# Kernel tuning notes

Measured on AMD Instinct MI355X. Metric: run time of the kernel, lower is better.

## Reference

```python
import jax, jax.numpy as jnp
import numpy as np

DIM = 1024
NUM_HEADS = 16
HEAD_DIM = DIM // NUM_HEADS
SCALE = 1.0 / float(np.sqrt(HEAD_DIM))


def setup_inputs() -> dict:
    key = jax.random.key(0)
    ks = jax.random.split(key, 8)
    b, n = 1, 4096
    x = jax.random.normal(ks[0], (b, n, DIM), dtype=jnp.float32)
    cos = jax.random.uniform(ks[1], (b, n, HEAD_DIM // 2), dtype=jnp.float32)
    sin = jax.random.uniform(ks[2], (b, n, HEAD_DIM // 2), dtype=jnp.float32)
    # qkv Linear(dim, 3*dim) and proj Linear(dim, dim); store weights as [in, out]
    w_qkv = jax.random.normal(ks[3], (DIM, 3 * DIM), dtype=jnp.float32) * (1.0 / np.sqrt(DIM))
    b_qkv = jax.random.normal(ks[4], (3 * DIM,), dtype=jnp.float32) * 0.01
    w_proj = jax.random.normal(ks[5], (DIM, DIM), dtype=jnp.float32) * (1.0 / np.sqrt(DIM))
    b_proj = jax.random.normal(ks[6], (DIM,), dtype=jnp.float32) * 0.01
    return {"x": x, "cos": cos, "sin": sin, "w_qkv": w_qkv, "b_qkv": b_qkv,
            "w_proj": w_proj, "b_proj": b_proj}


def _rotate_half(t):
    t1, t2 = jnp.split(t, 2, axis=-1)
    return jnp.concatenate([-t2, t1], axis=-1)


def reference(x, cos, sin, w_qkv, b_qkv, w_proj, b_proj):
    b, n, d = x.shape
    qkv = x @ w_qkv + b_qkv                      # [b, n, 3d]
    q, k, v = jnp.split(qkv, 3, axis=-1)
    # [b, n, h, hd] layout (avoids explicit transposes; einsum handles head axis)
    q = q.reshape(b, n, NUM_HEADS, HEAD_DIM)
    k = k.reshape(b, n, NUM_HEADS, HEAD_DIM)
    v = v.reshape(b, n, NUM_HEADS, HEAD_DIM)
    # RoPE: cos/sin [b, n, hd/2] -> [b, n, 1, hd], broadcast over heads
    cos_f = jnp.concatenate([cos, cos], axis=-1)[:, :, None, :]
    sin_f = jnp.concatenate([sin, sin], axis=-1)[:, :, None, :]
    q = q * cos_f + _rotate_half(q) * sin_f
    k = k * cos_f + _rotate_half(k) * sin_f
    # SDPA (non-causal, no dropout in eval)
    scores = jnp.einsum("bqhd,bkhd->bhqk", q, k) * SCALE
    attn = jax.nn.softmax(scores, axis=-1)
    out = jnp.einsum("bhqk,bkhd->bqhd", attn, v).reshape(b, n, d)
    return out @ w_proj + b_proj
```

## Files before the change

### kernel.cpp

```cpp
#include <hip/hip_runtime.h>
#include <hip/hip_bf16.h>
#include <cstdint>


#define TOK 4096
#define DIM_ 1024
#define NHEAD 16
#define HDIM 64
#define N3 3072
#define SCALE_LOG2E 0.18033688011112042f

typedef __bf16 bf16_t;
typedef bf16_t bf16x8 __attribute__((ext_vector_type(8)));
typedef float floatx4 __attribute__((ext_vector_type(4)));

__device__ __forceinline__ void async_ld16(const bf16_t* g, bf16_t* l) {
  __builtin_amdgcn_global_load_lds(
      (const __attribute__((address_space(1))) void*)(g),
      (__attribute__((address_space(3))) void*)(l), 16, 0, 0);
}

__global__ __launch_bounds__(256) void k_prep(
    const float* __restrict__ x, const float* __restrict__ w_qkv,
    const float* __restrict__ w_proj, bf16_t* __restrict__ xb,
    bf16_t* __restrict__ wqkvT, bf16_t* __restrict__ wprojT) {
  __shared__ float tile[32][33];
  const int b = blockIdx.x;
  if (b < 4096) {
    int i = b * 256 + threadIdx.x;
    float4 v = ((const float4*)x)[i];
    union { bf16_t bb[4]; uint64_t u; } p;
    p.bb[0] = (bf16_t)v.x; p.bb[1] = (bf16_t)v.y;
    p.bb[2] = (bf16_t)v.z; p.bb[3] = (bf16_t)v.w;
    ((uint64_t*)xb)[i] = p.u;
    return;
  }
  const float* in; bf16_t* out; int R, C, c0, r0;
  if (b < 7168) {
    int bb = b - 4096; in = w_qkv; out = wqkvT; R = 1024; C = 3072;
    c0 = (bb % 96) * 32; r0 = (bb / 96) * 32;
  } else {
    int bb = b - 7168; in = w_proj; out = wprojT; R = 1024; C = 1024;
    c0 = (bb % 32) * 32; r0 = (bb / 32) * 32;
  }
  int tx = threadIdx.x & 31, ty = threadIdx.x >> 5;
#pragma unroll
  for (int i = 0; i < 4; i++) {
    int r = ty + i * 8;
    tile[r][tx] = in[(size_t)(r0 + r) * C + c0 + tx];
  }
  __syncthreads();
#pragma unroll
  for (int i = 0; i < 4; i++) {
    int c = ty + i * 8;
    out[(size_t)(c0 + c) * R + r0 + tx] = (bf16_t)tile[tx][c];
  }
}

__global__ __launch_bounds__(256) void k_qkv(
    const bf16_t* __restrict__ A,
    const bf16_t* __restrict__ Bt,
    const float* __restrict__ bias,
    const float* __restrict__ cs,
    const float* __restrict__ sn,
    bf16_t* __restrict__ qb, bf16_t* __restrict__ kb, bf16_t* __restrict__ vT) {
  constexpr int K = 1024, BK = 32;
  __shared__ bf16_t As[128 * BK] __attribute__((aligned(16)));
  __shared__ bf16_t Bs[128 * BK] __attribute__((aligned(16)));
  const int t = threadIdx.x;
  const int lane = t & 63, w = t >> 6;
  const int lrow = lane & 15, quad = lane >> 4;
  const int m0 = blockIdx.y * 128, n0 = blockIdx.x * 128;
  const int wm = (w >> 1) * 64, wn = (w & 1) * 64;

  const floatx4 ZV = {0.f, 0.f, 0.f, 0.f};
  floatx4 acc[4][4];
#pragma unroll
  for (int i = 0; i < 4; i++)
#pragma unroll
    for (int j = 0; j < 4; j++) acc[i][j] = ZV;

  for (int kt = 0; kt < K; kt += BK) {
#pragma unroll
    for (int r = 0; r < 2; r++) {
      int idx = r * 256 + t;
      int lbase = (r * 256 + w * 64) * 8;
      async_ld16(&A[(size_t)(m0 + (idx >> 2)) * K + kt + (idx & 3) * 8], &As[lbase]);
      async_ld16(&Bt[(size_t)(n0 + (idx >> 2)) * K + kt + (idx & 3) * 8], &Bs[lbase]);
    }
    __syncthreads();
    bf16x8 af[4], bf[4];
#pragma unroll
    for (int i = 0; i < 4; i++)
      af[i] = *(const bf16x8*)&As[(wm + i * 16 + lrow) * BK + quad * 8];
#pragma unroll
    for (int i = 0; i < 4; i++)
      bf[i] = *(const bf16x8*)&Bs[(wn + i * 16 + lrow) * BK + quad * 8];
#pragma unroll
    for (int mi = 0; mi < 4; mi++)
#pragma unroll
      for (int ni = 0; ni < 4; ni++)
        acc[mi][ni] = __builtin_amdgcn_mfma_f32_16x16x32_bf16(af[mi], bf[ni], acc[mi][ni], 0, 0, 0);
    __syncthreads();
  }

  const int c0 = n0 + wn;
  const int seg = c0 >> 10;
  const int h = (c0 & 1023) >> 6;
  float bv[4];
#pragma unroll
  for (int ni = 0; ni < 4; ni++) bv[ni] = bias[c0 + ni * 16 + lrow];

  if (seg < 2) {
    bf16_t* base = ((seg == 0) ? qb : kb) + (size_t)h * TOK * HDIM;
    const float qs = (seg == 0) ? SCALE_LOG2E : 1.0f;
#pragma unroll
    for (int mi = 0; mi < 4; mi++) {
#pragma unroll
      for (int reg = 0; reg < 4; reg++) {
        const int r = m0 + wm + mi * 16 + quad * 4 + reg;
        const float c_lo = cs[r * 32 + lrow];
        const float c_hi = cs[r * 32 + 16 + lrow];
        const float s_lo = sn[r * 32 + lrow];
        const float s_hi = sn[r * 32 + 16 + lrow];
        const float v0 = acc[mi][0][reg] + bv[0];
        const float v1 = acc[mi][1][reg] + bv[1];
        const float v2 = acc[mi][2][reg] + bv[2];
        const float v3 = acc[mi][3][reg] + bv[3];
        const float o0 = (v0 * c_lo - v2 * s_lo) * qs;
        const float o1 = (v1 * c_hi - v3 * s_hi) * qs;
        const float o2 = (v2 * c_lo + v0 * s_lo) * qs;
        const float o3 = (v3 * c_hi + v1 * s_hi) * qs;
        bf16_t* rp = base + (size_t)r * HDIM + lrow;
        rp[0]  = (bf16_t)o0;
        rp[16] = (bf16_t)o1;
        rp[32] = (bf16_t)o2;
        rp[48] = (bf16_t)o3;
      }
    }
  } else {
    bf16_t* base = vT + (size_t)h * HDIM * TOK;
#pragma unroll
    for (int mi = 0; mi < 4; mi++) {
      const int rbase = m0 + wm + mi * 16 + quad * 4;
#pragma unroll
      for (int ni = 0; ni < 4; ni++) {
        union { bf16_t b[4]; uint64_t u; } p;
#pragma unroll
        for (int reg = 0; reg < 4; reg++) p.b[reg] = (bf16_t)(acc[mi][ni][reg] + bv[ni]);
        *(uint64_t*)&base[(size_t)(ni * 16 + lrow) * TOK + rbase] = p.u;
      }
    }
  }
}

__global__ __launch_bounds__(256, 4) void k_attn(
    const bf16_t* __restrict__ qb, const bf16_t* __restrict__ kb,
    const bf16_t* __restrict__ vT, bf16_t* __restrict__ ao) {
  __shared__ bf16_t Ks[2][64 * 64] __attribute__((aligned(16)));
  __shared__ bf16_t Ps[4][32 * 36] __attribute__((aligned(16)));
  const int t = threadIdx.x, lane = t & 63, w = t >> 6;
  const int lrow = lane & 15, quad = lane >> 4;
  const int qg = w & 1, kh = w >> 1;
  const int bx = blockIdx.x;
  const int h = ((bx & 7) << 1) | ((bx >> 3) & 1);
  const int q0 = (bx >> 4) * 64;
  const bf16_t* qh = qb + (size_t)h * TOK * HDIM;
  const bf16_t* khp = kb + (size_t)h * TOK * HDIM;
  const bf16_t* vhp = vT + (size_t)h * HDIM * TOK;
  bf16_t* Pw = &Ps[w][0];

  const int ksrc = (t >> 3) * HDIM + (((t & 7) ^ ((t >> 3) & 7)) * 8);

  bf16x8 qf[2][2];
#pragma unroll
  for (int ni = 0; ni < 2; ni++)
#pragma unroll
    for (int ks = 0; ks < 2; ks++)
      qf[ni][ks] = *(const bf16x8*)&qh[(size_t)(q0 + qg * 32 + ni * 16 + lrow) * HDIM + ks * 32 + quad * 8];

  const floatx4 ZV = {0.f, 0.f, 0.f, 0.f};
  floatx4 o[4][2];
  floatx4 lacc[2] = {ZV, ZV};
#pragma unroll
  for (int d = 0; d < 4; d++)
#pragma unroll
    for (int ni = 0; ni < 2; ni++) o[d][ni] = ZV;

#pragma unroll
  for (int r = 0; r < 2; r++)
    async_ld16(&khp[(size_t)(r * 32) * HDIM + ksrc], &Ks[0][r * 2048 + t * 8]);

  for (int it = 0; it < TOK / 64; ++it) {
    const int b = it & 1;
    __syncthreads();
    if (it + 1 < TOK / 64) {
      const size_t j1 = (size_t)(it + 1) * 64;
#pragma unroll
      for (int r = 0; r < 2; r++)
        async_ld16(&khp[(j1 + r * 32) * HDIM + ksrc], &Ks[b ^ 1][r * 2048 + t * 8]);
    }

    bf16x8 vf[4];
#pragma unroll
    for (int dt = 0; dt < 4; dt++)
      vf[dt] = *(const bf16x8*)&vhp[(size_t)(dt * 16 + lrow) * TOK + it * 64 + kh * 32 + quad * 8];

    floatx4 s[2][2];
#pragma unroll
    for (int mi = 0; mi < 2; mi++)
#pragma unroll
      for (int ni = 0; ni < 2; ni++) s[mi][ni] = ZV;
#pragma unroll
    for (int ks = 0; ks < 2; ks++)
#pragma unroll
      for (int mi = 0; mi < 2; mi++) {
        bf16x8 kf = *(const bf16x8*)&Ks[b][(kh * 32 + mi * 16 + lrow) * 64 + (((ks * 4 + quad) ^ (lrow & 7)) * 8)];
#pragma unroll
        for (int ni = 0; ni < 2; ni++)
          s[mi][ni] = __builtin_amdgcn_mfma_f32_16x16x32_bf16(kf, qf[ni][ks], s[mi][ni], 0, 0, 0);
      }

#pragma unroll
    for (int mi = 0; mi < 2; mi++)
#pragma unroll
      for (int ni = 0; ni < 2; ni++) {
#pragma unroll
        for (int reg = 0; reg < 4; reg++)
          s[mi][ni][reg] = __builtin_amdgcn_exp2f(s[mi][ni][reg]);
        lacc[ni] += s[mi][ni];
      }

#pragma unroll
    for (int mi = 0; mi < 2; mi++)
#pragma unroll
      for (int ni = 0; ni < 2; ni++) {
        union { bf16_t b4[4]; uint64_t u; } p;
#pragma unroll
        for (int reg = 0; reg < 4; reg++) p.b4[reg] = (bf16_t)s[mi][ni][reg];
        *(uint64_t*)&Pw[(ni * 16 + lrow) * 36 + (mi * 4 + quad) * 4] = p.u;
      }

    bf16x8 pf[2];
#pragma unroll
    for (int ni = 0; ni < 2; ni++) {
      const int row = (ni * 16 + lrow) * 36;
      union { uint64_t u[2]; bf16x8 v; } pp;
      pp.u[0] = *(const uint64_t*)&Pw[row + quad * 8];
      pp.u[1] = *(const uint64_t*)&Pw[row + quad * 8 + 4];
      pf[ni] = pp.v;
    }
#pragma unroll
    for (int dt = 0; dt < 4; dt++)
#pragma unroll
      for (int ni = 0; ni < 2; ni++)
        o[dt][ni] = __builtin_amdgcn_mfma_f32_16x16x32_bf16(vf[dt], pf[ni], o[dt][ni], 0, 0, 0);
  }

  __syncthreads();
  float* Mrg = (float*)&Ks[qg][0];
  float* Lmrg = (float*)&Ps[0][0];
  float lq[2];
#pragma unroll
  for (int ni = 0; ni < 2; ni++) {
    float l = lacc[ni][0] + lacc[ni][1] + lacc[ni][2] + lacc[ni][3];
    l += __shfl_xor(l, 16, 64);
    l += __shfl_xor(l, 32, 64);
    lq[ni] = l;
  }
  if (kh == 1) {
#pragma unroll
    for (int ni = 0; ni < 2; ni++) {
#pragma unroll
      for (int dt = 0; dt < 4; dt++)
        *(floatx4*)&Mrg[(ni * 16 + lrow) * 64 + dt * 16 + quad * 4] = o[dt][ni];
      if (quad == 0) Lmrg[qg * 32 + ni * 16 + lrow] = lq[ni];
    }
  }
  __syncthreads();
  if (kh == 0) {
#pragma unroll
    for (int ni = 0; ni < 2; ni++) {
      const float l = lq[ni] + Lmrg[qg * 32 + ni * 16 + lrow];
      const float inv = 1.0f / l;
      const int qrow = q0 + qg * 32 + ni * 16 + lrow;
#pragma unroll
      for (int dt = 0; dt < 4; dt++) {
        floatx4 ov = *(const floatx4*)&Mrg[(ni * 16 + lrow) * 64 + dt * 16 + quad * 4];
        union { bf16_t b4[4]; uint64_t u; } p;
#pragma unroll
        for (int reg = 0; reg < 4; reg++) p.b4[reg] = (bf16_t)((o[dt][ni][reg] + ov[reg]) * inv);
        *(uint64_t*)&ao[(size_t)qrow * DIM_ + h * HDIM + dt * 16 + quad * 4] = p.u;
      }
    }
  }
}

__global__ __launch_bounds__(256) void k_proj(
    const bf16_t* __restrict__ A,
    const bf16_t* __restrict__ Bt,
    const float* __restrict__ bias, float* __restrict__ out) {
  constexpr int K = 1024, BK = 32;
  __shared__ bf16_t As[64 * BK] __attribute__((aligned(16)));
  __shared__ bf16_t Bs[128 * BK] __attribute__((aligned(16)));
  const int t = threadIdx.x;
  const int lane = t & 63, w = t >> 6;
  const int lrow = lane & 15, quad = lane >> 4;
  const int m0 = blockIdx.y * 64, n0 = blockIdx.x * 128;
  const int wm = (w >> 1) * 32, wn = (w & 1) * 64;

  const floatx4 ZV = {0.f, 0.f, 0.f, 0.f};
  floatx4 acc[2][4];
#pragma unroll
  for (int i = 0; i < 2; i++)
#pragma unroll
    for (int j = 0; j < 4; j++) acc[i][j] = ZV;

  for (int kt = 0; kt < K; kt += BK) {
    async_ld16(&A[(size_t)(m0 + (t >> 2)) * K + kt + (t & 3) * 8], &As[w * 512]);
#pragma unroll
    for (int r = 0; r < 2; r++) {
      int idx = r * 256 + t;
      async_ld16(&Bt[(size_t)(n0 + (idx >> 2)) * K + kt + (idx & 3) * 8],
                 &Bs[(r * 256 + w * 64) * 8]);
    }
    __syncthreads();
    bf16x8 af[2], bf[4];
#pragma unroll
    for (int i = 0; i < 2; i++)
      af[i] = *(const bf16x8*)&As[(wm + i * 16 + lrow) * BK + quad * 8];
#pragma unroll
    for (int i = 0; i < 4; i++)
      bf[i] = *(const bf16x8*)&Bs[(wn + i * 16 + lrow) * BK + quad * 8];
#pragma unroll
    for (int mi = 0; mi < 2; mi++)
#pragma unroll
      for (int ni = 0; ni < 4; ni++)
        acc[mi][ni] = __builtin_amdgcn_mfma_f32_16x16x32_bf16(af[mi], bf[ni], acc[mi][ni], 0, 0, 0);
    __syncthreads();
  }

  const int c0 = n0 + wn;
#pragma unroll
  for (int ni = 0; ni < 4; ni++) {
    float bv = bias[c0 + ni * 16 + lrow];
#pragma unroll
    for (int mi = 0; mi < 2; mi++)
#pragma unroll
      for (int reg = 0; reg < 4; reg++) {
        int r = m0 + wm + mi * 16 + quad * 4 + reg;
        out[(size_t)r * DIM_ + c0 + ni * 16 + lrow] = acc[mi][ni][reg] + bv;
      }
  }
}

extern "C" void kernel_launch(void* const* d_in, const int* in_sizes, int n_in,
                              void* d_out, int out_size, void* d_ws, size_t ws_size,
                              hipStream_t stream) {
  const float* x      = (const float*)d_in[0];
  const float* cs     = (const float*)d_in[1];
  const float* sn     = (const float*)d_in[2];
  const float* w_qkv  = (const float*)d_in[3];
  const float* b_qkv  = (const float*)d_in[4];
  const float* w_proj = (const float*)d_in[5];
  const float* b_proj = (const float*)d_in[6];
  float* out = (float*)d_out;

  char* ws = (char*)d_ws;
  bf16_t* xb     = (bf16_t*)(ws);
  bf16_t* wqkvT  = (bf16_t*)(ws + 8388608);
  bf16_t* wprojT = (bf16_t*)(ws + 14680064);
  bf16_t* qb     = (bf16_t*)(ws + 16777216);
  bf16_t* kb     = (bf16_t*)(ws + 25165824);
  bf16_t* vT     = (bf16_t*)(ws + 33554432);
  bf16_t* ao     = xb;

  k_prep<<<dim3(8192), dim3(256), 0, stream>>>(x, w_qkv, w_proj, xb, wqkvT, wprojT);
  k_qkv<<<dim3(24, 32), dim3(256), 0, stream>>>(xb, wqkvT, b_qkv, cs, sn, qb, kb, vT);
  k_attn<<<dim3(1024), dim3(256), 0, stream>>>(qb, kb, vT, ao);
  k_proj<<<dim3(8, 64), dim3(256), 0, stream>>>(ao, wprojT, b_proj, out);
}
```

Before: 277.0 us.

## Stage V through LDS, swap P via permlane, software-pipeline PV MFMA

V tiles now go into double-buffered LDS with async global-to-LDS loads, the same way K tiles do, replacing direct per-lane global loads. The bf16 P fragment is rearranged into MFMA operand layout with permlane32/permlane16 swaps instead of a round trip through per-wave LDS scratch. The PV MFMA is deferred one iteration so it overlaps the next QK and exp work, with setprio raised around the MFMA blocks. The head-to-block mapping is also simplified. This adds LDS footprint and register pressure, which may lower occupancy.

```diff
diff --git a/kernel.cpp b/kernel.cpp
--- a/kernel.cpp
+++ b/kernel.cpp
@@ -18,6 +18,12 @@
   __builtin_amdgcn_global_load_lds(
       (const __attribute__((address_space(1))) void*)(g),
       (__attribute__((address_space(3))) void*)(l), 16, 0, 0);
+}
+
+__device__ __forceinline__ uint32_t pk2(float lo, float hi) {
+  union { bf16_t b[2]; uint32_t u; } p;
+  p.b[0] = (bf16_t)lo; p.b[1] = (bf16_t)hi;
+  return p.u;
 }
 
 __global__ __launch_bounds__(256) void k_prep(
@@ -158,19 +164,19 @@
     const bf16_t* __restrict__ qb, const bf16_t* __restrict__ kb,
     const bf16_t* __restrict__ vT, bf16_t* __restrict__ ao) {
   __shared__ bf16_t Ks[2][64 * 64] __attribute__((aligned(16)));
-  __shared__ bf16_t Ps[4][32 * 36] __attribute__((aligned(16)));
+  __shared__ bf16_t Vs[2][64 * 64] __attribute__((aligned(16)));
+  __shared__ float Lmrg[64];
   const int t = threadIdx.x, lane = t & 63, w = t >> 6;
   const int lrow = lane & 15, quad = lane >> 4;
   const int qg = w & 1, kh = w >> 1;
-  const int bx = blockIdx.x;
-  const int h = ((bx & 7) << 1) | ((bx >> 3) & 1);
-  const int q0 = (bx >> 4) * 64;
+  const int h = blockIdx.x & 15;
+  const int q0 = (blockIdx.x >> 4) * 64;
   const bf16_t* qh = qb + (size_t)h * TOK * HDIM;
   const bf16_t* khp = kb + (size_t)h * TOK * HDIM;
   const bf16_t* vhp = vT + (size_t)h * HDIM * TOK;
-  bf16_t* Pw = &Ps[w][0];
 
   const int ksrc = (t >> 3) * HDIM + (((t & 7) ^ ((t >> 3) & 7)) * 8);
+  const int vsrc = (t >> 3) * TOK + (((t & 7) ^ ((t >> 3) & 7)) * 8);
 
   bf16x8 qf[2][2];
 #pragma unroll
@@ -188,29 +194,42 @@
     for (int ni = 0; ni < 2; ni++) o[d][ni] = ZV;
 
 #pragma unroll
-  for (int r = 0; r < 2; r++)
+  for (int r = 0; r < 2; r++) {
     async_ld16(&khp[(size_t)(r * 32) * HDIM + ksrc], &Ks[0][r * 2048 + t * 8]);
+    async_ld16(&vhp[(size_t)(r * 32) * TOK + vsrc], &Vs[0][r * 2048 + t * 8]);
+  }
+
+  bf16x8 pf[2];
+  bf16x8 vf[4];
 
   for (int it = 0; it < TOK / 64; ++it) {
     const int b = it & 1;
     __syncthreads();
     if (it + 1 < TOK / 64) {
-      const size_t j1 = (size_t)(it + 1) * 64;
-#pragma unroll
-      for (int r = 0; r < 2; r++)
-        async_ld16(&khp[(j1 + r * 32) * HDIM + ksrc], &Ks[b ^ 1][r * 2048 + t * 8]);
-    }
-
-    bf16x8 vf[4];
-#pragma unroll
-    for (int dt = 0; dt < 4; dt++)
-      vf[dt] = *(const bf16x8*)&vhp[(size_t)(dt * 16 + lrow) * TOK + it * 64 + kh * 32 + quad * 8];
+      const int j1 = (it + 1) * 64;
+#pragma unroll
+      for (int r = 0; r < 2; r++) {
+        async_ld16(&khp[((size_t)j1 + r * 32) * HDIM + ksrc], &Ks[b ^ 1][r * 2048 + t * 8]);
+        async_ld16(&vhp[(size_t)(r * 32) * TOK + j1 + vsrc], &Vs[b ^ 1][r * 2048 + t * 8]);
+      }
+    }
+
+    if (it > 0) {
+      __builtin_amdgcn_s_setprio(1);
+#pragma unroll
+      for (int dt = 0; dt < 4; dt++)
+#pragma unroll
+        for (int ni = 0; ni < 2; ni++)
+          o[dt][ni] = __builtin_amdgcn_mfma_f32_16x16x32_bf16(vf[dt], pf[ni], o[dt][ni], 0, 0, 0);
+      __builtin_amdgcn_s_setprio(0);
+    }
 
     floatx4 s[2][2];
 #pragma unroll
     for (int mi = 0; mi < 2; mi++)
 #pragma unroll
       for (int ni = 0; ni < 2; ni++) s[mi][ni] = ZV;
+    __builtin_amdgcn_s_setprio(1);
 #pragma unroll
     for (int ks = 0; ks < 2; ks++)
 #pragma unroll
@@ -220,6 +239,11 @@
         for (int ni = 0; ni < 2; ni++)
           s[mi][ni] = __builtin_amdgcn_mfma_f32_16x16x32_bf16(kf, qf[ni][ks], s[mi][ni], 0, 0, 0);
       }
+    __builtin_amdgcn_s_setprio(0);
+
+#pragma unroll
+    for (int dt = 0; dt < 4; dt++)
+      vf[dt] = *(const bf16x8*)&Vs[b][(dt * 16 + lrow) * 64 + (((kh * 4 + quad) ^ (lrow & 7)) * 8)];
 
 #pragma unroll
     for (int mi = 0; mi < 2; mi++)
@@ -232,34 +256,29 @@
       }
 
 #pragma unroll
-    for (int mi = 0; mi < 2; mi++)
-#pragma unroll
-      for (int ni = 0; ni < 2; ni++) {
-        union { bf16_t b4[4]; uint64_t u; } p;
-#pragma unroll
-        for (int reg = 0; reg < 4; reg++) p.b4[reg] = (bf16_t)s[mi][ni][reg];
-        *(uint64_t*)&Pw[(ni * 16 + lrow) * 36 + (mi * 4 + quad) * 4] = p.u;
-      }
-
-    bf16x8 pf[2];
-#pragma unroll
     for (int ni = 0; ni < 2; ni++) {
-      const int row = (ni * 16 + lrow) * 36;
-      union { uint64_t u[2]; bf16x8 v; } pp;
-      pp.u[0] = *(const uint64_t*)&Pw[row + quad * 8];
-      pp.u[1] = *(const uint64_t*)&Pw[row + quad * 8 + 4];
+      uint32_t A0 = pk2(s[0][ni][0], s[0][ni][1]);
+      uint32_t A1 = pk2(s[0][ni][2], s[0][ni][3]);
+      uint32_t B0 = pk2(s[1][ni][0], s[1][ni][1]);
+      uint32_t B1 = pk2(s[1][ni][2], s[1][ni][3]);
+      auto u0 = __builtin_amdgcn_permlane32_swap(A0, B0, false, false);
+      auto u1 = __builtin_amdgcn_permlane32_swap(A1, B1, false, false);
+      auto c0 = __builtin_amdgcn_permlane16_swap(u0[0], u0[1], false, false);
+      auto c1 = __builtin_amdgcn_permlane16_swap(u1[0], u1[1], false, false);
+      union { uint32_t d[4]; bf16x8 v; } pp;
+      pp.d[0] = c0[0]; pp.d[1] = c1[0]; pp.d[2] = c0[1]; pp.d[3] = c1[1];
       pf[ni] = pp.v;
     }
-#pragma unroll
-    for (int dt = 0; dt < 4; dt++)
-#pragma unroll
-      for (int ni = 0; ni < 2; ni++)
-        o[dt][ni] = __builtin_amdgcn_mfma_f32_16x16x32_bf16(vf[dt], pf[ni], o[dt][ni], 0, 0, 0);
-  }
+  }
+
+#pragma unroll
+  for (int dt = 0; dt < 4; dt++)
+#pragma unroll
+    for (int ni = 0; ni < 2; ni++)
+      o[dt][ni] = __builtin_amdgcn_mfma_f32_16x16x32_bf16(vf[dt], pf[ni], o[dt][ni], 0, 0, 0);
 
   __syncthreads();
-  float* Mrg = (float*)&Ks[qg][0];
-  float* Lmrg = (float*)&Ps[0][0];
+  float* Mrg = (qg == 0) ? (float*)&Ks[0][0] : (float*)&Vs[0][0];
   float lq[2];
 #pragma unroll
   for (int ni = 0; ni < 2; ni++) {
```

Result: faster. 229.1 us (-17.3%).
